# Optimization experiments

Measured on AMD Instinct MI355X. Metric: run time of the kernel, lower is better.

Reference implementation:

```python
import jax, jax.numpy as jnp
import numpy as np

D_MODEL = 1024
N_HEADS = 16
LN_EPS = 1e-6  # flax LayerNorm default

def setup_inputs() -> dict:
    key = jax.random.key(0)
    k1, k2, k3 = jax.random.split(key, 3)
    B, S = 2, 2048
    x = jax.random.normal(k1, (B, S, D_MODEL), dtype=jnp.float32)
    W_qkv = jax.random.normal(k2, (D_MODEL, 3 * D_MODEL), dtype=jnp.float32) / np.sqrt(D_MODEL)
    W_out = jax.random.normal(k3, (D_MODEL, D_MODEL), dtype=jnp.float32) / np.sqrt(D_MODEL)
    q_scale = jnp.ones((D_MODEL,), dtype=jnp.float32)
    k_scale = jnp.ones((D_MODEL,), dtype=jnp.float32)
    return {"x": x, "W_qkv": W_qkv, "q_scale": q_scale, "k_scale": k_scale, "W_out": W_out}

def _layernorm(t, scale):
    mu = jnp.mean(t, axis=-1, keepdims=True)
    var = jnp.var(t, axis=-1, keepdims=True)
    return (t - mu) * jax.lax.rsqrt(var + LN_EPS) * scale

def reference(x, W_qkv, q_scale, k_scale, W_out):
    B, S, D = x.shape
    H = N_HEADS
    Hd = D // H
    # fused QKV projection (no bias)
    qkv = jnp.einsum('bsd,de->bse', x, W_qkv)
    q, k, v = jnp.split(qkv, 3, axis=-1)
    # QK-LayerNorm over full d_model (before head split), scale only
    q = _layernorm(q, q_scale)
    k = _layernorm(k, k_scale)
    # split heads: [b, s, h, hd]
    q = q.reshape(B, S, H, Hd)
    k = k.reshape(B, S, H, Hd)
    v = v.reshape(B, S, H, Hd)
    # eager attention with causal mask
    scores = jnp.einsum('bshd,bthd->bhst', q / jnp.sqrt(Hd).astype(q.dtype), k)  # [b,h,s,t]
    future = jnp.triu(jnp.ones((S, S), dtype=bool), 1)  # True on strictly-future positions
    scores = jnp.where(future[None, None, :, :], jnp.finfo(scores.dtype).min, scores)
    attn = jax.nn.softmax(scores, axis=-1)
    ctx = jnp.einsum('bhst,bthd->bshd', attn, v)
    out = jnp.einsum('bsd,de->bse', ctx.reshape(B, S, D), W_out)
    return out
```

## Files before the change

kernel.cpp:

```cpp
#include <hip/hip_runtime.h>
#include <cstdint>
#include <cstddef>

typedef __attribute__((ext_vector_type(8))) short short8;
typedef __attribute__((ext_vector_type(4))) float floatx4;

__device__ __forceinline__ float bf2f(unsigned short u) {
  union { unsigned int i; float f; } c; c.i = ((unsigned int)u) << 16; return c.f;
}
__device__ __forceinline__ unsigned short f2bf(float f) {
  union { float f; unsigned int i; } c; c.f = f;
  unsigned int r = c.i + 0x7fffu + ((c.i >> 16) & 1u);
  return (unsigned short)(r >> 16);
}
__device__ __forceinline__ unsigned int fbits(float f) {
  union { float f; unsigned int i; } c; c.f = f; return c.i;
}

__device__ __forceinline__ void glds16(const unsigned short* g, unsigned short* l) {
  __builtin_amdgcn_global_load_lds((const __attribute__((address_space(1))) void*)g,
                                   (__attribute__((address_space(3))) void*)l, 16, 0, 0);
}

__device__ __forceinline__ void tr_tile(const float* __restrict__ in,
                                        unsigned short* __restrict__ out,
                                        int R, int C, int bx, int by, int tid,
                                        unsigned short (*t)[33]) {
  const int cx = tid & 31, rl = tid >> 5;
#pragma unroll
  for (int i = 0; i < 4; ++i)
    t[rl + i * 8][cx] = f2bf(in[(size_t)(by * 32 + rl + i * 8) * C + bx * 32 + cx]);
  __syncthreads();
  const int oc = by * 32 + cx;
#pragma unroll
  for (int i = 0; i < 4; ++i)
    out[(size_t)(bx * 32 + rl + i * 8) * R + oc] = t[cx][rl + i * 8];
}

__global__ __launch_bounds__(256) void k_prep(const float* __restrict__ x,
                                              const float* __restrict__ Wq,
                                              const float* __restrict__ Wo,
                                              unsigned short* __restrict__ x_bf,
                                              unsigned short* __restrict__ WTq,
                                              unsigned short* __restrict__ WTo) {
  __shared__ unsigned short t[32][33];
  const int bid = blockIdx.x, tid = threadIdx.x;
  if (bid < 3072) {
    tr_tile(Wq, WTq, 1024, 3072, bid % 96, bid / 96, tid, t);
  } else if (bid < 4096) {
    int v = bid - 3072;
    tr_tile(Wo, WTo, 1024, 1024, v & 31, v >> 5, tid, t);
  } else {
    int i = (bid - 4096) * 256 + tid;
    float4 v = ((const float4*)x)[i];
    ushort4 o = { f2bf(v.x), f2bf(v.y), f2bf(v.z), f2bf(v.w) };
    ((ushort4*)x_bf)[i] = o;
  }
}

template <int MT, bool F32OUT>
__global__ __launch_bounds__(256) void k_gemm_bt(const unsigned short* __restrict__ A,
                                                 const unsigned short* __restrict__ BT,
                                                 void* __restrict__ Cout,
                                                 int M, int N, int K) {
  constexpr int NI = MT / 32;
  __shared__ unsigned short As[2][MT * 32];
  __shared__ unsigned short Bs[2][128 * 32];
  const int bm = blockIdx.x * MT, bn = blockIdx.y * 128;
  const int tid = threadIdx.x;
  const int wave = tid >> 6, lane = tid & 63;
  const int wm = (wave & 1) * (MT / 2), wn = (wave >> 1) * 64;
  const int lrow = lane & 15, lgrp = lane >> 4;
  floatx4 acc[NI][4] = {};

  const int lr4 = lane >> 2, lc8 = (lane & 3) * 8;
  const int br0 = wave * 32;
  const unsigned short* Bg0 = BT + (size_t)(bn + br0 + lr4) * K + lc8;
  const unsigned short* Bg1 = BT + (size_t)(bn + br0 + 16 + lr4) * K + lc8;
  const int ar0 = wave * (MT / 4);
  const unsigned short* Ag0 = A + (size_t)(bm + ar0 + lr4) * K + lc8;
  const unsigned short* Ag1 = A + (size_t)(bm + ar0 + 16 + lr4) * K + lc8;

  for (int k0 = 0; k0 < K; k0 += 64) {
#pragma unroll
    for (int u = 0; u < 2; ++u) {
      const int ko = k0 + u * 32;
      glds16(Ag0 + ko, &As[u][ar0 * 32]);
      if (MT == 128) glds16(Ag1 + ko, &As[u][(ar0 + 16) * 32]);
      glds16(Bg0 + ko, &Bs[u][br0 * 32]);
      glds16(Bg1 + ko, &Bs[u][(br0 + 16) * 32]);
    }
    __syncthreads();
#pragma unroll
    for (int u = 0; u < 2; ++u) {
      short8 a[NI], bfr[4];
#pragma unroll
      for (int i = 0; i < NI; ++i)
        a[i] = *(const short8*)&As[u][(wm + i * 16 + lrow) * 32 + lgrp * 8];
#pragma unroll
      for (int j = 0; j < 4; ++j)
        bfr[j] = *(const short8*)&Bs[u][(wn + j * 16 + lrow) * 32 + lgrp * 8];
#pragma unroll
      for (int i = 0; i < NI; ++i)
#pragma unroll
        for (int j = 0; j < 4; ++j)
          acc[i][j] = __builtin_amdgcn_mfma_f32_16x16x32_bf16(a[i], bfr[j], acc[i][j], 0, 0, 0);
    }
    __syncthreads();
  }
#pragma unroll
  for (int i = 0; i < NI; ++i)
#pragma unroll
    for (int j = 0; j < 4; ++j)
#pragma unroll
      for (int r = 0; r < 4; ++r) {
        int m = bm + wm + i * 16 + lgrp * 4 + r;
        int n = bn + wn + j * 16 + lrow;
        if (F32OUT)
          ((float*)Cout)[(size_t)m * N + n] = acc[i][j][r];
        else
          ((unsigned short*)Cout)[(size_t)m * N + n] = f2bf(acc[i][j][r]);
      }
}

__global__ __launch_bounds__(256) void k_lnv(const unsigned short* __restrict__ qkv,
                                             const float* __restrict__ q_scale,
                                             const float* __restrict__ k_scale,
                                             unsigned short* __restrict__ q_n,
                                             unsigned short* __restrict__ k_n,
                                             unsigned short* __restrict__ VT) {
  const int bid = blockIdx.x, tid = threadIdx.x;
  if (bid < 4096) {
    const int tok = bid;
    const int wave = tid >> 6, lane = tid & 63;
    __shared__ float red[2][4];
    const unsigned short* row = qkv + (size_t)tok * 3072;
#pragma unroll
    for (int seg = 0; seg < 2; ++seg) {
      const unsigned short* p  = row + seg * 1024;
      const float* sc = seg ? k_scale : q_scale;
      unsigned short* outp = (seg ? k_n : q_n) + (size_t)tok * 1024;
      ushort4 u = *(const ushort4*)&p[tid * 4];
      float xv[4] = { bf2f(u.x), bf2f(u.y), bf2f(u.z), bf2f(u.w) };
      float sum = xv[0] + xv[1] + xv[2] + xv[3];
      float sq  = xv[0]*xv[0] + xv[1]*xv[1] + xv[2]*xv[2] + xv[3]*xv[3];
      for (int off = 32; off; off >>= 1) {
        sum += __shfl_down(sum, off, 64);
        sq  += __shfl_down(sq,  off, 64);
      }
      if (lane == 0) { red[0][wave] = sum; red[1][wave] = sq; }
      __syncthreads();
      sum = red[0][0] + red[0][1] + red[0][2] + red[0][3];
      sq  = red[1][0] + red[1][1] + red[1][2] + red[1][3];
      __syncthreads();
      float mean = sum * (1.0f / 1024.0f);
      float var  = sq * (1.0f / 1024.0f) - mean * mean;
      float rstd = rsqrtf(var + 1e-6f);
      if (seg == 0) rstd *= 0.18033688011112042f;
      float4 su = *(const float4*)&sc[tid * 4];
      ushort4 o;
      o.x = f2bf((xv[0] - mean) * rstd * su.x);
      o.y = f2bf((xv[1] - mean) * rstd * su.y);
      o.z = f2bf((xv[2] - mean) * rstd * su.z);
      o.w = f2bf((xv[3] - mean) * rstd * su.w);
      *(ushort4*)&outp[tid * 4] = o;
    }
  } else {
    __shared__ unsigned short t[32][33];
    const int v = bid - 4096;
    const int bh = v & 31, b = bh >> 4, h = bh & 15;
    const int sy = (v >> 5) & 63, hx = v >> 11;
    const int cx = tid & 31, rl = tid >> 5;
#pragma unroll
    for (int i = 0; i < 4; ++i)
      t[rl + i * 8][cx] =
        qkv[(size_t)(b * 2048 + sy * 32 + rl + i * 8) * 3072 + 2048 + h * 64 + hx * 32 + cx];
    __syncthreads();
#pragma unroll
    for (int i = 0; i < 4; ++i)
      VT[((size_t)bh * 64 + hx * 32 + rl + i * 8) * 2048 + sy * 32 + cx] = t[cx][rl + i * 8];
  }
}


#define KS_STRIDE 72
#define VS_STRIDE 136
#define PS_STRIDE 136

#define MFMA_BF16 __builtin_amdgcn_mfma_f32_16x16x32_bf16

template <bool MASKED>
__device__ __forceinline__ void attn_step(int t0, int q0, int wq, int wt,
    const short8 (&qa)[2][2],
    const unsigned short* Ks, const unsigned short* Vs, unsigned short* Psq,
    floatx4 (&o)[2][4], floatx4 (&o_l)[2], int lrow, int lgrp) {
  const int twbase = wt * 64;
#pragma unroll
  for (int tb = 0; tb < 4; ++tb) {
    short8 kb0 = *(const short8*)&Ks[(twbase + tb * 16 + lrow) * KS_STRIDE + lgrp * 8];
    short8 kb1 = *(const short8*)&Ks[(twbase + tb * 16 + lrow) * KS_STRIDE + 32 + lgrp * 8];
#pragma unroll
    for (int qb = 0; qb < 2; ++qb) {
      floatx4 st = {};
      __builtin_amdgcn_s_setprio(1);
      st = MFMA_BF16(kb0, qa[qb][0], st, 0, 0, 0);
      st = MFMA_BF16(kb1, qa[qb][1], st, 0, 0, 0);
      __builtin_amdgcn_s_setprio(0);
      float p0 = exp2f(st[0]), p1 = exp2f(st[1]);
      float p2 = exp2f(st[2]), p3 = exp2f(st[3]);
      if (MASKED) {
        const int qcol = q0 + wq * 32 + qb * 16 + lrow;
        const int tbase = t0 + twbase + tb * 16 + lgrp * 4;
        p0 = (tbase     <= qcol) ? p0 : 0.0f;
        p1 = (tbase + 1 <= qcol) ? p1 : 0.0f;
        p2 = (tbase + 2 <= qcol) ? p2 : 0.0f;
        p3 = (tbase + 3 <= qcol) ? p3 : 0.0f;
      }
      uint2 pu;
      pu.x = __builtin_amdgcn_perm(fbits(p1), fbits(p0), 0x07060302u);
      pu.y = __builtin_amdgcn_perm(fbits(p3), fbits(p2), 0x07060302u);
      *(uint2*)&Psq[(qb * 16 + lrow) * PS_STRIDE + twbase + tb * 16 + lgrp * 4] = pu;
    }
  }
  const short8 vones = { 0x3F80, 0x3F80, 0x3F80, 0x3F80,
                         0x3F80, 0x3F80, 0x3F80, 0x3F80 };
#pragma unroll
  for (int kk = 0; kk < 2; ++kk) {
    short8 pa0 = *(const short8*)&Psq[lrow * PS_STRIDE + twbase + kk * 32 + lgrp * 8];
    short8 pa1 = *(const short8*)&Psq[(16 + lrow) * PS_STRIDE + twbase + kk * 32 + lgrp * 8];
    __builtin_amdgcn_s_setprio(1);
    o_l[0] = MFMA_BF16(pa0, vones, o_l[0], 0, 0, 0);
    o_l[1] = MFMA_BF16(pa1, vones, o_l[1], 0, 0, 0);
#pragma unroll
    for (int hb = 0; hb < 4; ++hb) {
      short8 vb = *(const short8*)&Vs[(hb * 16 + lrow) * VS_STRIDE + twbase + kk * 32 + lgrp * 8];
      o[0][hb] = MFMA_BF16(pa0, vb, o[0][hb], 0, 0, 0);
      o[1][hb] = MFMA_BF16(pa1, vb, o[1][hb], 0, 0, 0);
    }
    __builtin_amdgcn_s_setprio(0);
  }
}

__global__ __launch_bounds__(256) void k_flash(const unsigned short* __restrict__ q_n,
                                               const unsigned short* __restrict__ k_n,
                                               const unsigned short* __restrict__ VT,
                                               unsigned short* __restrict__ ctx) {
  const int S = 2048, D = 1024;
  const int bh = blockIdx.x, b = bh >> 4, h = bh & 15;
  const int qt = 31 - (int)blockIdx.y;
  const int q0 = qt * 64;
  const int tid = threadIdx.x, wave = tid >> 6, lane = tid & 63;
  const int wq = wave >> 1, wt = wave & 1;
  const int lrow = lane & 15, lgrp = lane >> 4;

  __shared__ __align__(16) unsigned char smem[53248];
  unsigned short* Ks  = (unsigned short*)smem;
  unsigned short* Vs  = (unsigned short*)(smem + 18432);
  unsigned short* Psq = (unsigned short*)(smem + 35840) + wq * 32 * PS_STRIDE;
  float* buf  = (float*)smem;
  float* Lbuf = (float*)(smem + 17408);

  const unsigned short* kg = k_n + (size_t)(b * S) * D + h * 64;
  const unsigned short* vg = VT + (size_t)bh * 64 * S;
  const int ksr = tid >> 3, ksc = (tid & 7) * 8;
  const int vsr = tid >> 4, vsc = (tid & 15) * 8;

  short8 qa[2][2];
#pragma unroll
  for (int qb = 0; qb < 2; ++qb) {
    const unsigned short* qp =
        q_n + (size_t)(b * S + q0 + wq * 32 + qb * 16 + lrow) * D + h * 64;
    qa[qb][0] = *(const short8*)(qp + lgrp * 8);
    qa[qb][1] = *(const short8*)(qp + 32 + lgrp * 8);
  }
  floatx4 o[2][4] = {};
  floatx4 o_l[2] = {};

  const int tend = q0 + 64;
  for (int t0 = 0; t0 < tend; t0 += 128) {
#pragma unroll
    for (int j = 0; j < 4; ++j) {
      int r = ksr + j * 32;
      *(int4*)&Ks[r * KS_STRIDE + ksc] = *(const int4*)(kg + (size_t)(t0 + r) * D + ksc);
    }
#pragma unroll
    for (int j = 0; j < 4; ++j) {
      int r = vsr + j * 16;
      *(int4*)&Vs[r * VS_STRIDE + vsc] = *(const int4*)(vg + (size_t)r * S + t0 + vsc);
    }
    __syncthreads();
    const bool half = (tend - t0) < 128;
    if (!(half && wt == 1)) {
      if (t0 + 128 <= q0)
        attn_step<false>(t0, q0, wq, wt, qa, Ks, Vs, Psq, o, o_l, lrow, lgrp);
      else
        attn_step<true>(t0, q0, wq, wt, qa, Ks, Vs, Psq, o, o_l, lrow, lgrp);
    }
    __syncthreads();
  }

  if (wt == 1) {
    if (lrow == 0) {
#pragma unroll
      for (int qb = 0; qb < 2; ++qb)
#pragma unroll
        for (int r = 0; r < 4; ++r)
          Lbuf[wq * 32 + qb * 16 + lgrp * 4 + r] = o_l[qb][r];
    }
    float* bf = buf + wq * 32 * 68;
#pragma unroll
    for (int qb = 0; qb < 2; ++qb)
#pragma unroll
      for (int hb = 0; hb < 4; ++hb)
#pragma unroll
        for (int r = 0; r < 4; ++r)
          bf[(qb * 16 + lgrp * 4 + r) * 68 + hb * 16 + lrow] = o[qb][hb][r];
  }
  __syncthreads();
  if (wt == 0) {
    float* bf = buf + wq * 32 * 68;
#pragma unroll
    for (int qb = 0; qb < 2; ++qb)
#pragma unroll
      for (int hb = 0; hb < 4; ++hb)
#pragma unroll
        for (int r = 0; r < 4; ++r)
          o[qb][hb][r] += bf[(qb * 16 + lgrp * 4 + r) * 68 + hb * 16 + lrow];
    unsigned short* op = ctx + (size_t)(b * S + q0 + wq * 32) * D + h * 64;
#pragma unroll
    for (int qb = 0; qb < 2; ++qb)
#pragma unroll
      for (int r = 0; r < 4; ++r) {
        float inv = 1.0f / (o_l[qb][r] + Lbuf[wq * 32 + qb * 16 + lgrp * 4 + r]);
        int row = qb * 16 + lgrp * 4 + r;
#pragma unroll
        for (int hb = 0; hb < 4; ++hb)
          op[(size_t)row * D + hb * 16 + lrow] = f2bf(o[qb][hb][r] * inv);
      }
  }
}

extern "C" void kernel_launch(void* const* d_in, const int* in_sizes, int n_in,
                              void* d_out, int out_size, void* d_ws, size_t ws_size,
                              hipStream_t stream) {
  const float* x       = (const float*)d_in[0];
  const float* W_qkv   = (const float*)d_in[1];
  const float* q_scale = (const float*)d_in[2];
  const float* k_scale = (const float*)d_in[3];
  const float* W_out   = (const float*)d_in[4];
  float* out = (float*)d_out;
  char* ws = (char*)d_ws;
  unsigned short* WT_qkv = (unsigned short*)(ws + 0);
  unsigned short* WT_out = (unsigned short*)(ws + 6291456);
  unsigned short* qkv    = (unsigned short*)(ws + 8388608);
  unsigned short* q_nb   = (unsigned short*)(ws + 33554432);
  unsigned short* k_nb   = (unsigned short*)(ws + 41943040);
  unsigned short* VT     = (unsigned short*)(ws + 50331648);
  unsigned short* x_bf   = (unsigned short*)(ws + 58720256);
  unsigned short* ctx    = qkv;

  k_prep<<<8192, 256, 0, stream>>>(x, W_qkv, W_out, x_bf, WT_qkv, WT_out);
  k_gemm_bt<128, false><<<dim3(32, 24), 256, 0, stream>>>(x_bf, WT_qkv, qkv, 4096, 3072, 1024);
  k_lnv<<<8192, 256, 0, stream>>>(qkv, q_scale, k_scale, q_nb, k_nb, VT);
  k_flash<<<dim3(32, 32), 256, 0, stream>>>(q_nb, k_nb, VT, ctx);
  k_gemm_bt<64, true><<<dim3(64, 8), 256, 0, stream>>>(ctx, WT_out, out, 4096, 1024, 1024);
}
```

Before: 182.6 us.

## Replace QKV GEMM with 256x256-tile 8-wave pipelined kernel using swizzled LDS

The QKV projection GEMM moves to a new kernel with 256x256 output tiles and 512 threads (8 waves). It double-buffers LDS with direct global-to-LDS loads, interleaves the next k-tiles' loads with MFMA phases under fine-grained vmcnt waits and barriers, and XOR-swizzles LDS columns to avoid bank conflicts. The goal is more operand reuse per load and better overlap of memory with matrix math than the old 128x128 kernel. The cost is 128KB of LDS per block, only 192 blocks (one wave of work on the GPU), and hardcoded shapes.

```diff
diff --git a/kernel.cpp b/kernel.cpp
--- a/kernel.cpp
+++ b/kernel.cpp
@@ -21,6 +21,8 @@
   __builtin_amdgcn_global_load_lds((const __attribute__((address_space(1))) void*)g,
                                    (__attribute__((address_space(3))) void*)l, 16, 0, 0);
 }
+
+#define MFMA_BF16 __builtin_amdgcn_mfma_f32_16x16x32_bf16
 
 __device__ __forceinline__ void tr_tile(const float* __restrict__ in,
                                         unsigned short* __restrict__ out,
@@ -58,6 +60,100 @@
   }
 }
 
+__global__ __launch_bounds__(512) void k_gemm8(const unsigned short* __restrict__ A,
+                                               const unsigned short* __restrict__ BT,
+                                               unsigned short* __restrict__ C) {
+  const int N = 3072, K = 1024;
+  const int bm = blockIdx.x * 256, bn = blockIdx.y * 256;
+  const int tid = threadIdx.x, wid = tid >> 6, lane = tid & 63;
+  const int wr = wid >> 2, wc = wid & 3;
+  const int lrow = lane & 15, lgrp = lane >> 4;
+
+  __shared__ unsigned short lds[65536];
+  unsigned short* Ab = lds;
+  unsigned short* Bb = lds + 32768;
+
+  const int srow = wid * 16 + (lane >> 2);
+  const int scb  = ((lane & 3) ^ ((lane >> 3) & 3)) * 8;
+  const unsigned short* aS = A  + (size_t)(bm + srow) * K + scb;
+  const unsigned short* bS = BT + (size_t)(bn + srow) * K + scb;
+  const int dst = wid * 512;
+
+#define STG_A(slot, t, h, kt) \
+  glds16(aS + (size_t)((h) * 128) * K + (kt) * 32, \
+         Ab + (slot) * 16384 + (t) * 8192 + (h) * 4096 + dst)
+#define STG_B(slot, t, h, kt) \
+  glds16(bS + (size_t)((h) * 128) * K + (kt) * 32, \
+         Bb + (slot) * 16384 + (t) * 8192 + (h) * 4096 + dst)
+
+  floatx4 acc[8][4] = {};
+  const int rsw = (lrow >> 1) & 3;
+
+  STG_A(0, 0, 0, 0); STG_A(0, 0, 1, 0); STG_B(0, 0, 0, 0); STG_B(0, 0, 1, 0);
+  STG_A(0, 1, 0, 1); STG_A(0, 1, 1, 1); STG_B(0, 1, 0, 1); STG_B(0, 1, 1, 1);
+  asm volatile("s_waitcnt vmcnt(4)" ::: "memory");
+  __builtin_amdgcn_s_barrier();
+
+  for (int i = 0; i < 16; ++i) {
+    const int cur = i & 1, nxt = cur ^ 1;
+    const int k2 = 2 * i + 2, k3 = 2 * i + 3;
+    const bool stg = (i < 15);
+    short8 bf[4];
+#pragma unroll
+    for (int p = 0; p < 8; ++p) {
+      const int t = p >> 2, q = p & 3;
+      short8 a0 = *(const short8*)&Ab[cur * 16384 + t * 8192 + wr * 4096 +
+                                      ((q * 2    ) * 16 + lrow) * 32 + (lgrp ^ rsw) * 8];
+      short8 a1 = *(const short8*)&Ab[cur * 16384 + t * 8192 + wr * 4096 +
+                                      ((q * 2 + 1) * 16 + lrow) * 32 + (lgrp ^ rsw) * 8];
+      if (q == 0) {
+#pragma unroll
+        for (int nj = 0; nj < 4; ++nj)
+          bf[nj] = *(const short8*)&Bb[cur * 16384 + t * 8192 + (wc >> 1) * 4096 +
+                                       ((wc & 1) * 64 + nj * 16 + lrow) * 32 +
+                                       (lgrp ^ rsw) * 8];
+      }
+      if (stg) {
+        if      (p == 0) STG_A(nxt, 0, 0, k2);
+        else if (p == 1) STG_A(nxt, 0, 1, k2);
+        else if (p == 2) STG_B(nxt, 0, 0, k2);
+        else if (p == 3) STG_B(nxt, 0, 1, k2);
+        else if (p == 4) STG_A(nxt, 1, 0, k3);
+        else if (p == 5) STG_A(nxt, 1, 1, k3);
+        else if (p == 6) STG_B(nxt, 1, 0, k3);
+        else             STG_B(nxt, 1, 1, k3);
+      }
+      if (p == 3) {
+        if (i < 15) asm volatile("s_waitcnt vmcnt(2)" ::: "memory");
+        else        asm volatile("s_waitcnt vmcnt(0)" ::: "memory");
+      }
+      if (p == 7)   asm volatile("s_waitcnt vmcnt(2)" ::: "memory");
+      __builtin_amdgcn_s_barrier();
+      __builtin_amdgcn_s_setprio(1);
+#pragma unroll
+      for (int nj = 0; nj < 4; ++nj) {
+        acc[q * 2    ][nj] = MFMA_BF16(a0, bf[nj], acc[q * 2    ][nj], 0, 0, 0);
+        acc[q * 2 + 1][nj] = MFMA_BF16(a1, bf[nj], acc[q * 2 + 1][nj], 0, 0, 0);
+      }
+      __builtin_amdgcn_s_setprio(0);
+      __builtin_amdgcn_s_barrier();
+    }
+  }
+#undef STG_A
+#undef STG_B
+
+#pragma unroll
+  for (int mi = 0; mi < 8; ++mi)
+#pragma unroll
+    for (int nj = 0; nj < 4; ++nj)
+#pragma unroll
+      for (int r = 0; r < 4; ++r) {
+        int m = bm + wr * 128 + mi * 16 + lgrp * 4 + r;
+        int n = bn + wc * 64 + nj * 16 + lrow;
+        C[(size_t)m * N + n] = f2bf(acc[mi][nj][r]);
+      }
+}
+
 template <int MT, bool F32OUT>
 __global__ __launch_bounds__(256) void k_gemm_bt(const unsigned short* __restrict__ A,
                                                  const unsigned short* __restrict__ BT,
@@ -104,7 +200,7 @@
       for (int i = 0; i < NI; ++i)
 #pragma unroll
         for (int j = 0; j < 4; ++j)
-          acc[i][j] = __builtin_amdgcn_mfma_f32_16x16x32_bf16(a[i], bfr[j], acc[i][j], 0, 0, 0);
+          acc[i][j] = MFMA_BF16(a[i], bfr[j], acc[i][j], 0, 0, 0);
     }
     __syncthreads();
   }
@@ -182,12 +278,9 @@
   }
 }
 
-
 #define KS_STRIDE 72
 #define VS_STRIDE 136
 #define PS_STRIDE 136
-
-#define MFMA_BF16 __builtin_amdgcn_mfma_f32_16x16x32_bf16
 
 template <bool MASKED>
 __device__ __forceinline__ void attn_step(int t0, int q0, int wq, int wt,
@@ -360,7 +453,7 @@
   unsigned short* ctx    = qkv;
 
   k_prep<<<8192, 256, 0, stream>>>(x, W_qkv, W_out, x_bf, WT_qkv, WT_out);
-  k_gemm_bt<128, false><<<dim3(32, 24), 256, 0, stream>>>(x_bf, WT_qkv, qkv, 4096, 3072, 1024);
+  k_gemm8<<<dim3(16, 12), 512, 0, stream>>>(x_bf, WT_qkv, qkv);
   k_lnv<<<8192, 256, 0, stream>>>(qkv, q_scale, k_scale, q_nb, k_nb, VT);
   k_flash<<<dim3(32, 32), 256, 0, stream>>>(q_nb, k_nb, VT, ctx);
   k_gemm_bt<64, true><<<dim3(64, 8), 256, 0, stream>>>(ctx, WT_out, out, 4096, 1024, 1024);
```

Measured after the change: 184.6 us. About the same (+1.1%).
